# Kernel optimization log

Hardware: AMD Instinct MI355X
Metric: run time of the kernel (lower is better)

Reference implementation:

```python
import jax, jax.numpy as jnp
import numpy as np


def _dnn(a, b):
    # tf.math.divide_no_nan
    safe = jnp.where(b == 0, 1.0, b)
    return jnp.where(b == 0, 0.0, a / safe)


def _safe_sqrt(x):
    # _sqrt: 0 where x == 0 (grad-safe)
    p = x > 0
    return jnp.where(p, jnp.sqrt(jnp.where(p, x, 1.0)), 0.0)


def _agg4(v):
    # mean/var/skew/kurt over last axis, using the sample skew/kurt formulas
    # from _skewness2/_kurtosis2 in the source.
    n = float(v.shape[-1])
    m = jnp.mean(v, -1)
    c = v - m[..., None]
    var = jnp.mean(c ** 2, -1)
    std = _safe_sqrt(var)
    skew = n / ((n - 1.0) * (n - 2.0)) * jnp.sum(_dnn(c, std[..., None]) ** 3, -1)
    k4 = jnp.sum(c ** 4, -1)
    k22 = jnp.sum(c ** 2, -1) ** 2
    alpha = n * (n + 1.0) * (n - 1.0) / (n - 2.0) / (n - 3.0)
    kurt = alpha * _dnn(k4, k22) - 3.0 * (n - 1.0) ** 2 / (n - 2.0) / (n - 3.0)
    return m, var, skew, kurt


def _forward(x):
    B, T, F = x.shape
    nT = float(T)

    mean = jnp.mean(x, 1)                        # [B,F]
    xc = x - mean[:, None, :]                    # x_sub_means
    var = jnp.mean(xc ** 2, 1)                   # population variance
    std = _safe_sqrt(var)
    # diff: conv kernel [0,1,-1] VALID -> d[t] = x[t+1] - x[t+2], len T-2
    xd = x[:, 1:-1, :] - x[:, 2:, :]
    xd_abs = jnp.abs(xd)

    scal = [mean,
            jnp.min(x, 1), jnp.max(x, 1),
            _safe_sqrt(jnp.mean(x ** 2, 1)),      # rms
            var, std]
    # skewness / kurtosis over time (exact formulas from source)
    skew = nT / ((nT - 1.0) * (nT - 2.0)) * jnp.sum(_dnn(xc, std[:, None, :]) ** 3, 1)
    k4 = jnp.sum(xc ** 4, 1)
    k22 = jnp.sum(xc ** 2, 1) ** 2
    alpha = nT * (nT + 1.0) * (nT - 1.0) / (nT - 2.0) / (nT - 3.0)
    kurt = alpha * _dnn(k4, k22) - 3.0 * (nT - 1.0) ** 2 / (nT - 2.0) / (nT - 3.0)
    scal += [skew, kurt,
             jnp.mean(xd, 1), jnp.sum(xd, 1), jnp.mean(xd_abs, 1),  # change stats
             jnp.sum(x ** 2, 1),                  # abs_energy
             jnp.max(jnp.abs(x), 1),              # abs_max
             jnp.sum(xd_abs, 1),                  # abs_sum_of_changes
             _safe_sqrt(jnp.sum(xd ** 2, 1))]     # cid_ce

    # quantiles (sorted) and time-based quantiles
    xs = jnp.sort(x, axis=1)
    q_idx = [round(p * T) for p in (0.25, 0.5, 0.75)]
    q = xs[:, q_idx, :]                           # [B,3,F]
    tb_idx = [min(round(p * T), T - 1) for p in (0.0, 0.25, 0.5, 0.75, 1.0)]
    tb = x[:, tb_idx, :]                          # [B,5,F]

    def count_above(sgn):
        # count_above_zero: T - count_nonzero(sign - 1) == #(sign == 1)
        return jnp.sum(sgn == 1, 1).astype(x.dtype)

    def crossings(sgn):
        return jnp.sum(sgn[:, 1:, :] != sgn[:, :-1, :], 1).astype(x.dtype)

    s_x = jnp.sign(x)
    s_c = jnp.sign(xc)
    s_tb = [jnp.sign(x - tb[:, i:i + 1, :]) for i in range(5)]
    s_q = [jnp.sign(x - q[:, i:i + 1, :]) for i in range(3)]

    scal += [count_above(s_x), count_above(s_c)] + [count_above(s) for s in s_tb]
    scal += [crossings(s_x), crossings(s_c)]
    scal += [crossings(s) for s in s_q]
    scal += [crossings(s) for s in s_tb]

    # FFT features
    fx = jnp.fft.rfft(x, axis=1)                  # [B, T//2+1, F]
    amp = jnp.transpose(jnp.abs(fx), (0, 2, 1))   # [B,F,nf]
    ang = jnp.transpose(jnp.angle(fx), (0, 2, 1))
    ratio = _dnn(amp, jnp.sum(amp, -1, keepdims=True))
    am, av, ask, aku = _agg4(amp)
    rm, rv, rsk, rku = _agg4(ratio)
    scal += [amp[:, :, 0], am, av, ask, aku, rm, rv, rsk, rku]

    # autocorrelation (lags 1..9), matching _autocorrelation:
    # ac[l] = sum_t xc[t]*xc[t+l] / (T - l) / variance
    lags = list(range(1, 10))
    ac = jnp.stack([_dnn(jnp.sum(xc[:, :T - l, :] * xc[:, l:, :], 1) / (nT - l), var)
                    for l in lags], axis=-1)      # [B,F,9]
    acm, acv, acs, ack = _agg4(ac)
    ac_rmax = _dnn(ac, jnp.max(ac, -1, keepdims=True))
    scal += [acm, acv, acs, ack]

    out = jnp.concatenate(
        [jnp.stack(scal, -1),                     # [B,F,45]
         jnp.transpose(q, (0, 2, 1)),             # [B,F,3]
         jnp.transpose(tb, (0, 2, 1)),            # [B,F,5]
         amp, ang, ratio,                         # [B,F,1025] each
         ac, ac_rmax], axis=-1)                   # [B,F,9] each
    return out                                    # [B,F,3146]


def setup_inputs() -> dict:
    key = jax.random.key(0)
    x = jax.random.normal(key, (512, 2048, 16), dtype=jnp.float32)
    return {"x": x}


def reference(x):
    return _forward(x)
```

## Files before the change

### kernel.cpp

```cpp
#include <hip/hip_runtime.h>
#include <math.h>

#define T_LEN 2048
#define NF    16
#define NTH   256
#define NOUT  3146
#define PI_F  3.14159265358979323846f

__device__ __forceinline__ float wred_sum(float v) {
  v += __shfl_down(v, 32); v += __shfl_down(v, 16); v += __shfl_down(v, 8);
  v += __shfl_down(v, 4);  v += __shfl_down(v, 2);  v += __shfl_down(v, 1);
  return v;
}
__device__ __forceinline__ float wred_min(float v) {
  v = fminf(v, __shfl_down(v, 32)); v = fminf(v, __shfl_down(v, 16)); v = fminf(v, __shfl_down(v, 8));
  v = fminf(v, __shfl_down(v, 4));  v = fminf(v, __shfl_down(v, 2));  v = fminf(v, __shfl_down(v, 1));
  return v;
}
__device__ __forceinline__ float wred_max(float v) {
  v = fmaxf(v, __shfl_down(v, 32)); v = fmaxf(v, __shfl_down(v, 16)); v = fmaxf(v, __shfl_down(v, 8));
  v = fmaxf(v, __shfl_down(v, 4));  v = fmaxf(v, __shfl_down(v, 2));  v = fmaxf(v, __shfl_down(v, 1));
  return v;
}

template<int N>
__device__ __forceinline__ void block_sum_n(float (&v)[N], float* redw, float* res, int tid) {
  const int wave = tid >> 6;
#pragma unroll
  for (int j = 0; j < N; j++) {
    float s = wred_sum(v[j]);
    if ((tid & 63) == 0) redw[j * 4 + wave] = s;
  }
  __syncthreads();
  if (tid < N) res[tid] = redw[tid * 4] + redw[tid * 4 + 1] + redw[tid * 4 + 2] + redw[tid * 4 + 3];
  __syncthreads();
}

__device__ __forceinline__ void agg4_9(const float* v, float* om, float* ov, float* os, float* ok) {
  const float fn = 9.0f;
  float s = 0.f;
#pragma unroll
  for (int i = 0; i < 9; i++) s += v[i];
  float m = s / fn;
  float c2 = 0.f, c3 = 0.f, c4 = 0.f;
#pragma unroll
  for (int i = 0; i < 9; i++) {
    float c = v[i] - m; float cc = c * c;
    c2 += cc; c3 += cc * c; c4 += cc * cc;
  }
  float var = c2 / fn;
  float sd = (var > 0.f) ? sqrtf(var) : 0.f;
  float sk = (sd > 0.f) ? fn / ((fn - 1.f) * (fn - 2.f)) * (c3 / (sd * sd * sd)) : 0.f;
  float k22 = c2 * c2;
  float al = fn * (fn + 1.f) * (fn - 1.f) / ((fn - 2.f) * (fn - 3.f));
  float ku = ((k22 > 0.f) ? al * c4 / k22 : 0.f)
             - 3.f * (fn - 1.f) * (fn - 1.f) / ((fn - 2.f) * (fn - 3.f));
  *om = m; *ov = var; *os = sk; *ok = ku;
}

__device__ __forceinline__ float ord2f(unsigned int u) {
  unsigned int v = (u & 0x80000000u) ? (u ^ 0x80000000u) : ~u;
  return __uint_as_float(v);
}
__device__ __forceinline__ unsigned int f2ord(float v) {
  unsigned int u = __float_as_uint(v);
  return (u & 0x80000000u) ? ~u : (u | 0x80000000u);
}

__device__ __forceinline__ float fast_atan2f(float y, float x) {
  float ay = fabsf(y), ax = fabsf(x);
  float mx = fmaxf(ax, ay), mn = fminf(ax, ay);
  if (mx == 0.f) return 0.f;
  float t = __fdividef(mn, mx);
  float s = t * t;
  float p = fmaf(s, fmaf(s, fmaf(s, fmaf(s, 0.0208351f, -0.0851330f), 0.1801410f), -0.3302995f), 0.9998660f);
  float r = t * p;
  if (ay > ax) r = 1.57079632679f - r;
  if (x < 0.f) r = PI_F - r;
  return (y < 0.f) ? -r : r;
}

__global__ __launch_bounds__(NTH)
void ts_feat_kernel(const float* __restrict__ x, float* __restrict__ out, int gpx) {
  __shared__ __align__(16) float a[T_LEN];
  __shared__ __align__(16) unsigned int U[2048];
  __shared__ float redw[96];
  __shared__ float res[24];
  __shared__ unsigned int selres[8];

  float* zr = a;
  float* zi = a + 1024;
  float* Tc = (float*)U;
  float* Ts = (float*)U + 1024;

  const int tid = threadIdx.x;
  const int lane = tid & 63;
  const int wave = tid >> 6;
  int b, f;
  {
    int i = blockIdx.x;
    if (gpx > 0) { int xc = i & 7; int slot = i >> 3; b = xc * gpx + (slot >> 4); f = slot & 15; }
    else { b = i >> 4; f = i & 15; }
  }
  const float* xp = x + ((size_t)b * T_LEN) * NF + f;
  float* op = out + (size_t)(b * NF + f) * NOUT;
  const float fT = (float)T_LEN;

#pragma unroll
  for (int k = 0; k < 5; k++) U[tid + k * NTH] = 0u;

  unsigned int key[8];
  float s1 = 0.f, s2 = 0.f, s3 = 0.f, s4 = 0.f, mn = 3.4e38f, mx = -3.4e38f;
#pragma unroll
  for (int k = 0; k < 8; k++) {
    int t = tid + k * NTH;
    float v = xp[(size_t)t * NF];
    a[t] = v;
    key[k] = f2ord(v);
    float v2 = v * v;
    s1 += v; s2 += v2; s3 += v2 * v; s4 += v2 * v2;
    mn = fminf(mn, v); mx = fmaxf(mx, v);
  }
  s1 = wred_sum(s1); s2 = wred_sum(s2); s3 = wred_sum(s3); s4 = wred_sum(s4);
  mn = wred_min(mn); mx = wred_max(mx);
  if (lane == 0) {
    redw[wave] = s1; redw[4 + wave] = s2; redw[8 + wave] = s3; redw[12 + wave] = s4;
    redw[16 + wave] = mn; redw[20 + wave] = mx;
  }
  __syncthreads();

  const int woff = wave << 8;
#pragma unroll
  for (int k = 0; k < 8; k++) atomicAdd(&U[woff + (key[k] >> 24)], 1u);
  if (tid == 0) {
    res[0] = redw[0] + redw[1] + redw[2] + redw[3];
    res[1] = redw[4] + redw[5] + redw[6] + redw[7];
    res[2] = redw[8] + redw[9] + redw[10] + redw[11];
    res[3] = redw[12] + redw[13] + redw[14] + redw[15];
    res[4] = fminf(fminf(redw[16], redw[17]), fminf(redw[18], redw[19]));
    res[5] = fmaxf(fmaxf(redw[20], redw[21]), fmaxf(redw[22], redw[23]));
  }
  __syncthreads();

  float S1 = res[0], S2v = res[1], S3v = res[2], S4v = res[3], MN = res[4], MX = res[5];
  float mean = S1 / fT;
  float maxabs = fmaxf(-MN, MX);
  float rms = sqrtf(fmaxf(S2v / fT, 0.f));

  if (tid < 64) {
    const int l = tid;
    unsigned int b0 = U[4*l]   + U[256+4*l]   + U[512+4*l]   + U[768+4*l];
    unsigned int b1 = U[4*l+1] + U[256+4*l+1] + U[512+4*l+1] + U[768+4*l+1];
    unsigned int b2 = U[4*l+2] + U[256+4*l+2] + U[512+4*l+2] + U[768+4*l+2];
    unsigned int b3 = U[4*l+3] + U[256+4*l+3] + U[512+4*l+3] + U[768+4*l+3];
    unsigned int t0 = b0, t1 = t0 + b1, t2 = t1 + b2, t3 = t2 + b3;
    unsigned int tot = t3;
#pragma unroll
    for (int off = 1; off < 64; off <<= 1) {
      unsigned int n = __shfl_up(tot, off);
      if (l >= off) tot += n;
    }
    unsigned int base0 = tot - t3;
    U[1024+4*l] = base0+t0; U[1024+4*l+1] = base0+t1; U[1024+4*l+2] = base0+t2; U[1024+4*l+3] = base0+t3;
  }

  float v13[13];
  {
    const int base = tid * 8;
    const float4* a4 = (const float4*)a;
    float4 w0 = a4[tid*2], w1 = a4[tid*2+1];
    int i2 = (base + 11 < T_LEN) ? tid*2+2 : 0;
    int i3 = (base + 15 < T_LEN) ? tid*2+3 : 0;
    float4 w2 = a4[i2], w3 = a4[i3];
    bool ok2 = (base + 11 < T_LEN), ok3 = (base + 15 < T_LEN);
    float r[17];
    r[0]=w0.x; r[1]=w0.y; r[2]=w0.z; r[3]=w0.w;
    r[4]=w1.x; r[5]=w1.y; r[6]=w1.z; r[7]=w1.w;
    r[8]  = ok2 ? w2.x : mean; r[9]  = ok2 ? w2.y : mean; r[10] = ok2 ? w2.z : mean; r[11] = ok2 ? w2.w : mean;
    r[12] = ok3 ? w3.x : mean; r[13] = ok3 ? w3.y : mean; r[14] = ok3 ? w3.z : mean; r[15] = ok3 ? w3.w : mean;
    r[16] = (base + 16 < T_LEN) ? a[base + 16] : mean;
#pragma unroll
    for (int j = 0; j < 13; j++) v13[j] = 0.f;
#pragma unroll
    for (int j = 0; j < 8; j++) {
      if (base + j < T_LEN - 2) {
        float d = r[j+1] - r[j+2];
        v13[0] += d; v13[1] += fabsf(d); v13[2] += d * d;
      }
    }
#pragma unroll
    for (int l = 1; l <= 9; l++) {
#pragma unroll
      for (int j = 0; j < 8; j++) {
        v13[2 + l] += (r[j] - mean) * (r[j + l] - mean);
      }
    }
#pragma unroll
    for (int j = 0; j < 8; j++) {
      float c = r[j] - mean;
      v13[12] += c * c;
    }
  }
  __syncthreads();

  unsigned int prefix[3];
  unsigned int rank[3];
  {
    unsigned int incl = U[1024 + tid];
    unsigned int excl = (tid == 0) ? 0u : U[1024 + tid - 1];
    const unsigned int rks[3] = {512u, 1024u, 1536u};
#pragma unroll
    for (int j = 0; j < 3; j++)
      if (excl <= rks[j] && rks[j] < incl) { selres[2*j] = (unsigned)tid; selres[2*j+1] = rks[j] - excl; }
    U[tid] = 0u; U[tid + 256] = 0u; U[tid + 512] = 0u;
  }

  block_sum_n<13>(v13, redw, res, tid);
  float SD = res[0], SAD = res[1], SDD = res[2];
  float C2w = res[12];
  float var = C2w / fT;
  float sd = (var > 0.f) ? sqrtf(var) : 0.f;
  float C3 = S3v - 3.f*mean*S2v + 2.f*fT*mean*mean*mean;
  float mm = mean * mean;
  float C4 = S4v - 4.f*mean*S3v + 6.f*mm*S2v - 3.f*fT*mm*mm;
  float skw = (sd > 0.f) ? (fT / ((fT - 1.f) * (fT - 2.f))) * (C3 / (sd * sd * sd)) : 0.f;
  float k22 = C2w * C2w;
  float alphaT = fT * (fT + 1.f) * (fT - 1.f) / ((fT - 2.f) * (fT - 3.f));
  float kurt = ((k22 > 0.f) ? alphaT * C4 / k22 : 0.f)
               - 3.f * (fT - 1.f) * (fT - 1.f) / ((fT - 2.f) * (fT - 3.f));
  float ac[9], acm, acv, acs, ack, acmax;
  {
    float invvar = (var != 0.f) ? 1.f / var : 0.f;
#pragma unroll
    for (int l = 1; l <= 9; l++) ac[l-1] = res[2 + l] / (fT - (float)l) * invvar;
    agg4_9(ac, &acm, &acv, &acs, &ack);
    acmax = ac[0];
#pragma unroll
    for (int l = 1; l < 9; l++) acmax = fmaxf(acmax, ac[l]);
  }
#pragma unroll
  for (int j = 0; j < 3; j++) { prefix[j] = selres[2*j] << 24; rank[j] = selres[2*j+1]; }

  for (int rnd = 1; rnd < 4; rnd++) {
    const int shift = 24 - 8 * rnd;
#pragma unroll
    for (int k = 0; k < 8; k++) {
      unsigned int u = key[k];
      unsigned int hi = u >> (shift + 8);
#pragma unroll
      for (int j = 0; j < 3; j++) {
        if (hi == (prefix[j] >> (shift + 8)))
          atomicAdd(&U[j * 256 + ((u >> shift) & 255u)], 1u);
      }
    }
    __syncthreads();
    if (tid < 192) {
      int w = tid >> 6, l = tid & 63;
      unsigned int* h = U + w * 256;
      unsigned int b0 = h[4*l], b1 = h[4*l+1], b2 = h[4*l+2], b3 = h[4*l+3];
      unsigned int t0 = b0, t1 = t0+b1, t2 = t1+b2, t3 = t2+b3;
      unsigned int tot = t3;
#pragma unroll
      for (int off = 1; off < 64; off <<= 1) {
        unsigned int n = __shfl_up(tot, off);
        if (l >= off) tot += n;
      }
      unsigned int base0 = tot - t3;
      unsigned int* c = U + 768 + w * 256;
      c[4*l] = base0+t0; c[4*l+1] = base0+t1; c[4*l+2] = base0+t2; c[4*l+3] = base0+t3;
    }
    __syncthreads();
    if (tid < 192) {
      int j = tid >> 6, l = tid & 63;
#pragma unroll
      for (int i = 0; i < 4; i++) {
        int bk = 4 * l + i;
        unsigned int incl = U[768 + j * 256 + bk];
        unsigned int excl = (bk == 0) ? 0u : U[768 + j * 256 + bk - 1];
        if (excl <= rank[j] && rank[j] < incl) { selres[2*j] = (unsigned)bk; selres[2*j+1] = rank[j] - excl; }
      }
    } else if (rnd < 3) {
      int z0 = (tid - 192) * 12;
#pragma unroll
      for (int k = 0; k < 12; k++) U[z0 + k] = 0u;
    }
    __syncthreads();
#pragma unroll
    for (int j = 0; j < 3; j++) { prefix[j] |= selres[2*j] << shift; rank[j] = selres[2*j+1]; }
  }
  float q0 = ord2f(prefix[0]), q1 = ord2f(prefix[1]), q2 = ord2f(prefix[2]);
  float tb0 = a[0], tb1 = a[512], tb2 = a[1024], tb3 = a[1536], tb4 = a[2047];

  {
    const unsigned int kt0 = f2ord(0.f), kt1 = f2ord(mean), kt2 = prefix[0], kt3 = prefix[1], kt4 = prefix[2];
    const unsigned int kt5 = f2ord(tb0), kt6 = f2ord(tb1), kt7 = f2ord(tb2), kt8 = f2ord(tb3), kt9 = f2ord(tb4);
    int cnt0=0,cnt1=0,cnt2=0,cnt3=0,cnt4=0,cnt5=0,cnt6=0,cnt7=0,cnt8=0,cnt9=0;
    int crs0=0,crs1=0,crs2=0,crs3=0,crs4=0,crs5=0,crs6=0,crs7=0,crs8=0,crs9=0;
#pragma unroll
    for (int k = 0; k < 8; k++) {
      unsigned int kv = key[k];
#define BAL(J, KT)                                                        \
      { unsigned long long mp = __ballot(kv > (KT));                      \
        unsigned long long mz = __ballot(kv == (KT));                     \
        cnt##J += (int)__popcll(mp);                                      \
        unsigned long long df = ((mp ^ (mp >> 1)) | (mz ^ (mz >> 1)))     \
                                & 0x7fffffffffffffffull;                  \
        crs##J += (int)__popcll(df); }
      BAL(0, kt0) BAL(1, kt1) BAL(2, kt2) BAL(3, kt3) BAL(4, kt4)
      BAL(5, kt5) BAL(6, kt6) BAL(7, kt7) BAL(8, kt8) BAL(9, kt9)
#undef BAL
    }
    if (tid < 64) {
      unsigned long long pk = 0ull;
      if (tid < 31) {
        float a0 = a[64*tid + 63], a1 = a[64*tid + 64];
#define SEAMB(J, TH)                                                      \
        { bool g0 = a0 > (TH), g1 = a1 > (TH);                            \
          bool e0 = a0 == (TH), e1 = a1 == (TH);                          \
          if ((g0 != g1) || (e0 != e1)) pk |= (1ull << (6*(J))); }
        SEAMB(0, 0.f) SEAMB(1, mean) SEAMB(2, q0) SEAMB(3, q1) SEAMB(4, q2)
        SEAMB(5, tb0) SEAMB(6, tb1) SEAMB(7, tb2) SEAMB(8, tb3) SEAMB(9, tb4)
#undef SEAMB
      }
      pk += __shfl_down(pk, 32); pk += __shfl_down(pk, 16); pk += __shfl_down(pk, 8);
      pk += __shfl_down(pk, 4);  pk += __shfl_down(pk, 2);  pk += __shfl_down(pk, 1);
      if (tid == 0) {
#pragma unroll
        for (int j = 0; j < 10; j++) redw[80 + j] = (float)((unsigned int)((pk >> (6*j)) & 63ull));
      }
    }
    if (lane == 0) {
      int w20 = wave * 20;
      redw[w20+0]=(float)cnt0; redw[w20+1]=(float)cnt1; redw[w20+2]=(float)cnt2;
      redw[w20+3]=(float)cnt3; redw[w20+4]=(float)cnt4; redw[w20+5]=(float)cnt5;
      redw[w20+6]=(float)cnt6; redw[w20+7]=(float)cnt7; redw[w20+8]=(float)cnt8;
      redw[w20+9]=(float)cnt9;
      redw[w20+10]=(float)crs0; redw[w20+11]=(float)crs1; redw[w20+12]=(float)crs2;
      redw[w20+13]=(float)crs3; redw[w20+14]=(float)crs4; redw[w20+15]=(float)crs5;
      redw[w20+16]=(float)crs6; redw[w20+17]=(float)crs7; redw[w20+18]=(float)crs8;
      redw[w20+19]=(float)crs9;
    }
  }

  {
    float cs, sn;
    __sincosf(-PI_F * (float)tid * (1.f / 256.f), &sn, &cs);
    const float cd = 0.9999952938095762f;
    const float sd_ = -0.0030679567629659761f;
#pragma unroll
    for (int j = 0; j < 4; j++) {
      int k = 4 * tid + j;
      int xk = k ^ (k >> 5);
      Tc[xk] = cs; Ts[xk] = sn;
      float ncs = cs * cd - sn * sd_;
      float nsn = sn * cd + cs * sd_;
      cs = ncs; sn = nsn;
    }
  }

  float2 rz0, rz1, rz2, rz3;
  {
    const float2* a2 = (const float2*)a;
    rz0 = a2[tid]; rz1 = a2[tid + 256]; rz2 = a2[tid + 512]; rz3 = a2[tid + 768];
  }
  __syncthreads();

  if (tid < 20) {
    float s = redw[tid] + redw[20 + tid] + redw[40 + tid] + redw[60 + tid];
    if (tid >= 10) s += redw[80 + (tid - 10)];
    res[4 + tid] = s;
  }
  {
#define SCAT(K, Z)                                                     \
    { int p = tid + (K) * 256;                                         \
      int rl = (int)(__brev((unsigned)(p & 31)) >> 27);                \
      int c = p >> 5;                                                  \
      int idx = rl * 32 + (c ^ rl);                                    \
      zr[idx] = (Z).x; zi[idx] = (Z).y; }
    SCAT(0, rz0) SCAT(1, rz1) SCAT(2, rz2) SCAT(3, rz3)
#undef SCAT
  }
  __syncthreads();
  float gr[4], gi[4];
#pragma unroll
  for (int k = 0; k < 4; k++) {
    int m = tid + k * 256;
    int h = m >> 5, l = m & 31;
    int rl5 = (int)(__brev((unsigned)l) >> 27);
    int idx = h * 32 + (rl5 ^ h);
    gr[k] = zr[idx]; gi[k] = zi[idx];
  }
  __syncthreads();
#pragma unroll
  for (int k = 0; k < 4; k++) { int m = tid + k * 256; zr[m] = gr[k]; zi[m] = gi[k]; }
  __syncthreads();

  {
    float4 R = ((const float4*)zr)[tid];
    float4 I = ((const float4*)zi)[tid];
    float u0r = R.x + R.y, u0i = I.x + I.y;
    float u1r = R.x - R.y, u1i = I.x - I.y;
    float u2r = R.z + R.w, u2i = I.z + I.w;
    float u3r = R.z - R.w, u3i = I.z - I.w;
    float4 Ro, Io;
    Ro.x = u0r + u2r; Io.x = u0i + u2i;
    Ro.z = u0r - u2r; Io.z = u0i - u2i;
    Ro.y = u1r + u3i; Io.y = u1i - u3r;
    Ro.w = u1r - u3i; Io.w = u1i + u3r;
    ((float4*)zr)[tid] = Ro; ((float4*)zi)[tid] = Io;
  }
#pragma unroll
  for (int p = 1; p < 5; p++) {
    const int hf = 1 << (2 * p);
    __syncthreads();
    const int qq = tid & (hf - 1);
    const int i0 = ((tid >> (2 * p)) << (2 * p + 2)) | qq;
    const int i1 = i0 + hf, i2 = i0 + 2 * hf, i3 = i0 + 3 * hf;
    const int t1 = qq << (10 - 2 * p);
    const int t2 = qq << (9 - 2 * p);
    const int t3 = t2 + 512;
    const int x1 = t1 ^ (t1 >> 5), x2 = t2 ^ (t2 >> 5), x3 = t3 ^ (t3 >> 5);
    float cA = Tc[x1], sA = Ts[x1];
    float cB = Tc[x2], sB = Ts[x2];
    float cC = Tc[x3], sC = Ts[x3];
    float r0 = zr[i0], m0 = zi[i0], r1 = zr[i1], m1 = zi[i1];
    float r2 = zr[i2], m2 = zi[i2], r3 = zr[i3], m3 = zi[i3];
    float a1r = cA*r1 - sA*m1, a1i = cA*m1 + sA*r1;
    float a3r = cA*r3 - sA*m3, a3i = cA*m3 + sA*r3;
    float u0r = r0 + a1r, u0i = m0 + a1i;
    float u1r = r0 - a1r, u1i = m0 - a1i;
    float u2r = r2 + a3r, u2i = m2 + a3i;
    float u3r = r2 - a3r, u3i = m2 - a3i;
    float b2r = cB*u2r - sB*u2i, b2i = cB*u2i + sB*u2r;
    float b3r = cC*u3r - sC*u3i, b3i = cC*u3i + sC*u3r;
    zr[i0] = u0r + b2r; zi[i0] = u0i + b2i;
    zr[i2] = u0r - b2r; zi[i2] = u0i - b2i;
    zr[i1] = u1r + b3r; zi[i1] = u1i + b3i;
    zr[i3] = u1r - b3r; zi[i3] = u1i - b3i;
  }
  __syncthreads();

  float ampv[4], angv[4];
  float v4[4] = {0.f, 0.f, 0.f, 0.f};
#pragma unroll
  for (int k = 0; k < 4; k++) {
    int kk = tid + k * NTH;
    int nk = (1024 - kk) & 1023;
    float z1r = zr[kk], z1i = zi[kk];
    float z2r = zr[nk], z2i = zi[nk];
    float Er = 0.5f * (z1r + z2r), Ei = 0.5f * (z1i - z2i);
    float Or = 0.5f * (z1i + z2i), Oi = -0.5f * (z1r - z2r);
    int xk = kk ^ (kk >> 5);
    float cs = Tc[xk], sn = Ts[xk];
    float Xr = Er + cs * Or - sn * Oi;
    float Xi = Ei + cs * Oi + sn * Or;
    float amp = sqrtf(Xr * Xr + Xi * Xi);
    ampv[k] = amp;
    angv[k] = fast_atan2f(Xi, Xr);
    float a2p = amp * amp;
    v4[0] += amp; v4[1] += a2p; v4[2] += a2p * amp; v4[3] += a2p * a2p;
  }
  float amp4 = 0.f, ang4 = 0.f;
  if (tid == 0) {
    float Xr = zr[0] - zi[0];
    amp4 = fabsf(Xr);
    ang4 = (Xr < 0.f) ? PI_F : 0.f;
    float a2p = amp4 * amp4;
    v4[0] += amp4; v4[1] += a2p; v4[2] += a2p * amp4; v4[3] += a2p * a2p;
  }
  block_sum_n<4>(v4, redw, res, tid);
  float S = res[0], M2 = res[1], M3 = res[2], M4 = res[3];
  const float fn = 1025.f;
  float am = S / fn;
  float A2 = M2 - fn * am * am;
  float A3 = M3 - 3.f * am * M2 + 2.f * fn * am * am * am;
  float am2 = am * am;
  float A4 = M4 - 4.f * am * M3 + 6.f * am2 * M2 - 3.f * fn * am2 * am2;
  float av = A2 / fn;
  float asd = (av > 0.f) ? sqrtf(av) : 0.f;
  float ask = (asd > 0.f) ? fn / ((fn - 1.f) * (fn - 2.f)) * (A3 / (asd * asd * asd)) : 0.f;
  float ak22 = A2 * A2;
  float aal = fn * (fn + 1.f) * (fn - 1.f) / ((fn - 2.f) * (fn - 3.f));
  float aku = ((ak22 > 0.f) ? aal * A4 / ak22 : 0.f)
              - 3.f * (fn - 1.f) * (fn - 1.f) / ((fn - 2.f) * (fn - 3.f));
  float invS = (S != 0.f) ? 1.f / S : 0.f;
  float rm = am * invS;
  float rv = av * invS * invS;

#pragma unroll
  for (int k = 0; k < 4; k++) {
    int kk = tid + k * NTH;
    op[53 + kk]   = ampv[k];
    op[1078 + kk] = angv[k];
    op[2103 + kk] = ampv[k] * invS;
  }
  if (tid < 9) {
    float acj;
    switch (tid) {
      case 0: acj = ac[0]; break; case 1: acj = ac[1]; break; case 2: acj = ac[2]; break;
      case 3: acj = ac[3]; break; case 4: acj = ac[4]; break; case 5: acj = ac[5]; break;
      case 6: acj = ac[6]; break; case 7: acj = ac[7]; break; default: acj = ac[8]; break;
    }
    op[3128 + tid] = acj;
    op[3137 + tid] = (acmax != 0.f) ? acj / acmax : 0.f;
  }
  if (tid == 0) {
    op[53 + 1024] = amp4; op[1078 + 1024] = ang4; op[2103 + 1024] = amp4 * invS;
    op[0] = mean; op[1] = MN; op[2] = MX; op[3] = rms; op[4] = var; op[5] = sd;
    op[6] = skw; op[7] = kurt;
    op[8] = SD / (fT - 2.f); op[9] = SD; op[10] = SAD / (fT - 2.f);
    op[11] = S2v; op[12] = maxabs; op[13] = SAD;
    op[14] = (SDD > 0.f) ? sqrtf(SDD) : 0.f;
    op[15] = res[4]; op[16] = res[5];
    op[17] = res[9]; op[18] = res[10]; op[19] = res[11]; op[20] = res[12]; op[21] = res[13];
    op[22] = res[14]; op[23] = res[15];
    op[24] = res[16]; op[25] = res[17]; op[26] = res[18];
    op[27] = res[19]; op[28] = res[20]; op[29] = res[21]; op[30] = res[22]; op[31] = res[23];
    op[32] = ampv[0];
    op[33] = am; op[34] = av; op[35] = ask; op[36] = aku;
    op[37] = rm; op[38] = rv; op[39] = ask; op[40] = aku;
    op[41] = acm; op[42] = acv; op[43] = acs; op[44] = ack;
    op[45] = q0; op[46] = q1; op[47] = q2;
    op[48] = tb0; op[49] = tb1; op[50] = tb2; op[51] = tb3; op[52] = tb4;
  }
}

extern "C" void kernel_launch(void* const* d_in, const int* in_sizes, int n_in,
                              void* d_out, int out_size, void* d_ws, size_t ws_size,
                              hipStream_t stream) {
  const float* x = (const float*)d_in[0];
  float* out = (float*)d_out;
  const int total = in_sizes[0];
  const int B = total / (T_LEN * NF);
  const int nblocks = B * NF;
  const int gpx = (B % 8 == 0) ? (B / 8) : 0;
  ts_feat_kernel<<<nblocks, NTH, 0, stream>>>(x, out, gpx);
}
```

Before: 204.2 us.

## Swizzle FFT shared-memory layout, shorten atan polynomial, hoist centered values

Applies an XOR swizzle (ZPHYS) to the zr/zi shared arrays used by the FFT stages, scatter, gather and post-processing, to cut LDS bank conflicts in the strided butterfly accesses. It also replaces the degree-9 atan polynomial with a lower-degree one, reducing ALU work per output angle but lowering the accuracy of the phase output. Separately, centered values r[j]-mean are computed once instead of being recomputed inside the autocorrelation loop.

```diff
diff --git a/kernel.cpp b/kernel.cpp
--- a/kernel.cpp
+++ b/kernel.cpp
@@ -6,6 +6,8 @@
 #define NTH   256
 #define NOUT  3146
 #define PI_F  3.14159265358979323846f
+
+#define ZPHYS(i) ((i) ^ ((((i) >> 5) & 7) << 2))
 
 __device__ __forceinline__ float wred_sum(float v) {
   v += __shfl_down(v, 32); v += __shfl_down(v, 16); v += __shfl_down(v, 8);
@@ -73,7 +75,7 @@
   if (mx == 0.f) return 0.f;
   float t = __fdividef(mn, mx);
   float s = t * t;
-  float p = fmaf(s, fmaf(s, fmaf(s, fmaf(s, 0.0208351f, -0.0851330f), 0.1801410f), -0.3302995f), 0.9998660f);
+  float p = fmaf(s, fmaf(s, 0.079331f, -0.288679f), 0.995354f);
   float r = t * p;
   if (ay > ax) r = 1.57079632679f - r;
   if (x < 0.f) r = PI_F - r;
@@ -179,6 +181,9 @@
     r[8]  = ok2 ? w2.x : mean; r[9]  = ok2 ? w2.y : mean; r[10] = ok2 ? w2.z : mean; r[11] = ok2 ? w2.w : mean;
     r[12] = ok3 ? w3.x : mean; r[13] = ok3 ? w3.y : mean; r[14] = ok3 ? w3.z : mean; r[15] = ok3 ? w3.w : mean;
     r[16] = (base + 16 < T_LEN) ? a[base + 16] : mean;
+    float cw[17];
+#pragma unroll
+    for (int j = 0; j < 17; j++) cw[j] = r[j] - mean;
 #pragma unroll
     for (int j = 0; j < 13; j++) v13[j] = 0.f;
 #pragma unroll
@@ -192,14 +197,11 @@
     for (int l = 1; l <= 9; l++) {
 #pragma unroll
       for (int j = 0; j < 8; j++) {
-        v13[2 + l] += (r[j] - mean) * (r[j + l] - mean);
-      }
-    }
-#pragma unroll
-    for (int j = 0; j < 8; j++) {
-      float c = r[j] - mean;
-      v13[12] += c * c;
-    }
+        v13[2 + l] += cw[j] * cw[j + l];
+      }
+    }
+#pragma unroll
+    for (int j = 0; j < 8; j++) v13[12] += cw[j] * cw[j];
   }
   __syncthreads();
 
@@ -376,7 +378,8 @@
       int rl = (int)(__brev((unsigned)(p & 31)) >> 27);                \
       int c = p >> 5;                                                  \
       int idx = rl * 32 + (c ^ rl);                                    \
-      zr[idx] = (Z).x; zi[idx] = (Z).y; }
+      int px = ZPHYS(idx);                                             \
+      zr[px] = (Z).x; zi[px] = (Z).y; }
     SCAT(0, rz0) SCAT(1, rz1) SCAT(2, rz2) SCAT(3, rz3)
 #undef SCAT
   }
@@ -388,16 +391,22 @@
     int h = m >> 5, l = m & 31;
     int rl5 = (int)(__brev((unsigned)l) >> 27);
     int idx = h * 32 + (rl5 ^ h);
-    gr[k] = zr[idx]; gi[k] = zi[idx];
-  }
-  __syncthreads();
-#pragma unroll
-  for (int k = 0; k < 4; k++) { int m = tid + k * 256; zr[m] = gr[k]; zi[m] = gi[k]; }
-  __syncthreads();
-
-  {
-    float4 R = ((const float4*)zr)[tid];
-    float4 I = ((const float4*)zi)[tid];
+    int px = ZPHYS(idx);
+    gr[k] = zr[px]; gi[k] = zi[px];
+  }
+  __syncthreads();
+#pragma unroll
+  for (int k = 0; k < 4; k++) {
+    int m = tid + k * 256;
+    int px = ZPHYS(m);
+    zr[px] = gr[k]; zi[px] = gi[k];
+  }
+  __syncthreads();
+
+  {
+    int qt = tid ^ ((tid >> 3) & 7);
+    float4 R = ((const float4*)zr)[qt];
+    float4 I = ((const float4*)zi)[qt];
     float u0r = R.x + R.y, u0i = I.x + I.y;
     float u1r = R.x - R.y, u1i = I.x - I.y;
     float u2r = R.z + R.w, u2i = I.z + I.w;
@@ -407,7 +416,7 @@
     Ro.z = u0r - u2r; Io.z = u0i - u2i;
     Ro.y = u1r + u3i; Io.y = u1i - u3r;
     Ro.w = u1r - u3i; Io.w = u1i + u3r;
-    ((float4*)zr)[tid] = Ro; ((float4*)zi)[tid] = Io;
+    ((float4*)zr)[qt] = Ro; ((float4*)zi)[qt] = Io;
   }
 #pragma unroll
   for (int p = 1; p < 5; p++) {
@@ -416,6 +425,7 @@
     const int qq = tid & (hf - 1);
     const int i0 = ((tid >> (2 * p)) << (2 * p + 2)) | qq;
     const int i1 = i0 + hf, i2 = i0 + 2 * hf, i3 = i0 + 3 * hf;
+    const int p0 = ZPHYS(i0), p1 = ZPHYS(i1), p2x = ZPHYS(i2), p3x = ZPHYS(i3);
     const int t1 = qq << (10 - 2 * p);
     const int t2 = qq << (9 - 2 * p);
     const int t3 = t2 + 512;
@@ -423,8 +433,8 @@
     float cA = Tc[x1], sA = Ts[x1];
     float cB = Tc[x2], sB = Ts[x2];
     float cC = Tc[x3], sC = Ts[x3];
-    float r0 = zr[i0], m0 = zi[i0], r1 = zr[i1], m1 = zi[i1];
-    float r2 = zr[i2], m2 = zi[i2], r3 = zr[i3], m3 = zi[i3];
+    float r0 = zr[p0], m0 = zi[p0], r1 = zr[p1], m1 = zi[p1];
+    float r2 = zr[p2x], m2 = zi[p2x], r3 = zr[p3x], m3 = zi[p3x];
     float a1r = cA*r1 - sA*m1, a1i = cA*m1 + sA*r1;
     float a3r = cA*r3 - sA*m3, a3i = cA*m3 + sA*r3;
     float u0r = r0 + a1r, u0i = m0 + a1i;
@@ -433,10 +443,10 @@
     float u3r = r2 - a3r, u3i = m2 - a3i;
     float b2r = cB*u2r - sB*u2i, b2i = cB*u2i + sB*u2r;
     float b3r = cC*u3r - sC*u3i, b3i = cC*u3i + sC*u3r;
-    zr[i0] = u0r + b2r; zi[i0] = u0i + b2i;
-    zr[i2] = u0r - b2r; zi[i2] = u0i - b2i;
-    zr[i1] = u1r + b3r; zi[i1] = u1i + b3i;
-    zr[i3] = u1r - b3r; zi[i3] = u1i - b3i;
+    zr[p0] = u0r + b2r; zi[p0] = u0i + b2i;
+    zr[p2x] = u0r - b2r; zi[p2x] = u0i - b2i;
+    zr[p1] = u1r + b3r; zi[p1] = u1i + b3i;
+    zr[p3x] = u1r - b3r; zi[p3x] = u1i - b3i;
   }
   __syncthreads();
 
@@ -446,8 +456,9 @@
   for (int k = 0; k < 4; k++) {
     int kk = tid + k * NTH;
     int nk = (1024 - kk) & 1023;
-    float z1r = zr[kk], z1i = zi[kk];
-    float z2r = zr[nk], z2i = zi[nk];
+    int pk_ = ZPHYS(kk), pn_ = ZPHYS(nk);
+    float z1r = zr[pk_], z1i = zi[pk_];
+    float z2r = zr[pn_], z2i = zi[pn_];
     float Er = 0.5f * (z1r + z2r), Ei = 0.5f * (z1i - z2i);
     float Or = 0.5f * (z1i + z2i), Oi = -0.5f * (z1r - z2r);
     int xk = kk ^ (kk >> 5);
```

After: 202.8 us. No clear change (-0.7%).
